# Performance work log

Measured on AMD Instinct MI355X. Metric: run time of the kernel, lower is better.

Reference implementation:

```python
import jax, jax.numpy as jnp
import numpy as np

N, D, O, E = 100000, 32, 64, 1600000

def setup_inputs() -> dict:
    key = jax.random.key(0)
    ks = jax.random.split(key, 6)
    x = jax.random.normal(ks[0], (N, D), dtype=jnp.float32)
    edge_index = jax.random.randint(ks[1], (2, E), 0, N, dtype=jnp.int64)
    edge_attr = jax.random.uniform(ks[2], (E, 1), dtype=jnp.float32)
    # nodec MLP params (stored as [in, out]; equiv to torch Linear weight.T)
    W1 = jax.random.normal(ks[3], (3 * D, O), dtype=jnp.float32) * (1.0 / np.sqrt(3 * D))
    b1 = jnp.zeros((O,), dtype=jnp.float32)
    W2 = jax.random.normal(ks[4], (O, O), dtype=jnp.float32) * (1.0 / np.sqrt(O))
    b2 = jnp.zeros((O,), dtype=jnp.float32)
    return {"x": x, "edge_index": edge_index, "edge_attr": edge_attr,
            "W1": W1, "b1": b1, "W2": W2, "b2": b2}

def reference(x, edge_index, edge_attr, W1, b1, W2, b2):
    row, col = edge_index[0], edge_index[1]
    n = x.shape[0]
    # gather, weight by edge_attr, scatter-add into destination nodes
    mi = jax.ops.segment_sum(edge_attr * x[row], col, num_segments=n)  # [N, D]
    mo = jax.ops.segment_sum(edge_attr * x[col], row, num_segments=n)  # [N, D]
    M = jnp.concatenate([mi, mo, x], axis=-1)  # [N, 3D]
    h = jnp.tanh(M @ W1 + b1)
    return jnp.tanh(h @ W2 + b2)
```

## Files before the change

### kernel.cpp

```cpp
#include <hip/hip_runtime.h>
#include <hip/hip_bf16.h>


#define DFEAT 32
#define OFEAT 64
#define EPB   2048
#define KEYS_PER_BIN 128
#define NBINMAX 1568
#define CAP   3072

typedef unsigned long long u64;

__device__ __forceinline__ float rdlane(float v, int l) {
    return __int_as_float(__builtin_amdgcn_readlane(__float_as_int(v), l));
}

__global__ __launch_bounds__(512) void hist_part(
    const int* __restrict__ ei, int* __restrict__ blockhist, int E, int NBIN)
{
    __shared__ int lh[NBINMAX];
    int blk = blockIdx.x, tid = threadIdx.x;
    for (int i = tid; i < NBIN; i += 512) lh[i] = 0;
    __syncthreads();
    int e0 = blk * EPB;
    if (e0 + EPB <= E) {
        int4 rr = *(const int4*)(ei + e0 + tid * 4);
        int4 cc = *(const int4*)(ei + E + e0 + tid * 4);
        atomicAdd(&lh[(2 * cc.x) >> 7], 1); atomicAdd(&lh[(2 * rr.x + 1) >> 7], 1);
        atomicAdd(&lh[(2 * cc.y) >> 7], 1); atomicAdd(&lh[(2 * rr.y + 1) >> 7], 1);
        atomicAdd(&lh[(2 * cc.z) >> 7], 1); atomicAdd(&lh[(2 * rr.z + 1) >> 7], 1);
        atomicAdd(&lh[(2 * cc.w) >> 7], 1); atomicAdd(&lh[(2 * rr.w + 1) >> 7], 1);
    } else {
        #pragma unroll
        for (int j = 0; j < 4; ++j) {
            int e = e0 + tid * 4 + j;
            if (e < E) {
                atomicAdd(&lh[(2 * ei[E + e]) >> 7], 1);
                atomicAdd(&lh[(2 * ei[e] + 1) >> 7], 1);
            }
        }
    }
    __syncthreads();
    for (int i = tid; i < NBIN; i += 512)
        blockhist[(long long)blk * NBIN + i] = lh[i];
}

__global__ __launch_bounds__(64) void colscan(
    const int* __restrict__ blockhist, int* __restrict__ ofsT,
    int* __restrict__ bintotal, int nPB, int NBIN)
{
    int bin  = blockIdx.x;
    int lane = threadIdx.x;
    int run = 0;
    for (int b0 = 0; b0 < nPB; b0 += 64) {
        int b = b0 + lane;
        int v = (b < nPB) ? blockhist[(long long)b * NBIN + bin] : 0;
        int s = v;
        #pragma unroll
        for (int d = 1; d < 64; d <<= 1) {
            int t = __shfl_up(s, d, 64);
            if (lane >= d) s += t;
        }
        if (b < nPB) ofsT[(long long)bin * nPB + b] = s - v + run;
        run += __shfl(s, 63, 64);
    }
    if (lane == 0) bintotal[bin] = run;
}

__global__ __launch_bounds__(1024) void scan_bins(
    const int* __restrict__ bintotal, int* __restrict__ binbase, int NBIN)
{
    __shared__ int s[1024];
    int t = threadIdx.x;
    int i0 = 2 * t, i1 = 2 * t + 1;
    int p0 = (i0 < NBIN) ? ((bintotal[i0] + 1) & ~1) : 0;
    int p1 = (i1 < NBIN) ? ((bintotal[i1] + 1) & ~1) : 0;
    int v = p0 + p1;
    s[t] = v;
    __syncthreads();
    for (int o = 1; o < 1024; o <<= 1) {
        int u = (t >= o) ? s[t - o] : 0;
        __syncthreads();
        s[t] += u;
        __syncthreads();
    }
    int excl = s[t] - v;
    if (i0 < NBIN) binbase[i0] = excl;
    if (i1 < NBIN) binbase[i1] = excl + p0;
}

__global__ __launch_bounds__(512) void partition_kernel(
    const int* __restrict__ ei, const float* __restrict__ ea,
    const int* __restrict__ ofsT, const int* __restrict__ binbase,
    u64* __restrict__ pay, int E, int NBIN, int nPB)
{
    __shared__ unsigned short lofsw[NBINMAX + 1];
    __shared__ int lcur[NBINMAX];
    __shared__ int lbase[NBINMAX];
    __shared__ u64 stag[2 * EPB];
    int blk = blockIdx.x, tid = threadIdx.x;
    int e0 = blk * EPB;

    for (int i = tid; i < NBIN; i += 512) lcur[i] = 0;
    __syncthreads();

    int4 rr, cc; float4 av; bool full = (e0 + EPB <= E);
    if (full) {
        rr = *(const int4*)(ei + e0 + tid * 4);
        cc = *(const int4*)(ei + E + e0 + tid * 4);
        av = *(const float4*)(ea + e0 + tid * 4);
        atomicAdd(&lcur[(2 * cc.x) >> 7], 1); atomicAdd(&lcur[(2 * rr.x + 1) >> 7], 1);
        atomicAdd(&lcur[(2 * cc.y) >> 7], 1); atomicAdd(&lcur[(2 * rr.y + 1) >> 7], 1);
        atomicAdd(&lcur[(2 * cc.z) >> 7], 1); atomicAdd(&lcur[(2 * rr.z + 1) >> 7], 1);
        atomicAdd(&lcur[(2 * cc.w) >> 7], 1); atomicAdd(&lcur[(2 * rr.w + 1) >> 7], 1);
    } else {
        int rs[4], cs[4]; float as[4];
        #pragma unroll
        for (int j = 0; j < 4; ++j) {
            int e = e0 + tid * 4 + j;
            if (e < E) {
                rs[j] = ei[e]; cs[j] = ei[E + e]; as[j] = ea[e];
                atomicAdd(&lcur[(2 * cs[j]) >> 7], 1);
                atomicAdd(&lcur[(2 * rs[j] + 1) >> 7], 1);
            } else { rs[j] = 0; cs[j] = 0; as[j] = 0.0f; }
        }
        rr = make_int4(rs[0], rs[1], rs[2], rs[3]);
        cc = make_int4(cs[0], cs[1], cs[2], cs[3]);
        av = make_float4(as[0], as[1], as[2], as[3]);
    }
    __syncthreads();

    if (tid < 64) {
        int runc = 0;
        for (int b0 = 0; b0 < NBIN; b0 += 64) {
            int i = b0 + tid;
            int v = (i < NBIN) ? lcur[i] : 0;
            int s = v;
            #pragma unroll
            for (int d = 1; d < 64; d <<= 1) {
                int t2 = __shfl_up(s, d, 64);
                if (tid >= d) s += t2;
            }
            if (i < NBIN) lofsw[i] = (unsigned short)(s - v + runc);
            runc += __shfl(s, 63, 64);
        }
        if (tid == 0) lofsw[NBIN] = (unsigned short)runc;
    }
    __syncthreads();

    for (int i = tid; i < NBIN; i += 512) {
        lcur[i] = 0;
        lbase[i] = binbase[i] + ofsT[(long long)i * nPB + blk];
    }
    __syncthreads();

    {
        int rs[4] = {rr.x, rr.y, rr.z, rr.w};
        int cs[4] = {cc.x, cc.y, cc.z, cc.w};
        float as[4] = {av.x, av.y, av.z, av.w};
        #pragma unroll
        for (int j = 0; j < 4; ++j) {
            int e = e0 + tid * 4 + j;
            if (e < E) {
                unsigned int ab = (unsigned int)__float_as_int(as[j]);
                {
                    int key = 2 * cs[j]; int bin = key >> 7;
                    int t2 = atomicAdd(&lcur[bin], 1);
                    stag[(int)lofsw[bin] + t2] = ((u64)ab << 32) |
                        (unsigned int)(rs[j] | ((key & 127) << 17));
                }
                {
                    int key = 2 * rs[j] + 1; int bin = key >> 7;
                    int t2 = atomicAdd(&lcur[bin], 1);
                    stag[(int)lofsw[bin] + t2] = ((u64)ab << 32) |
                        (unsigned int)(cs[j] | ((key & 127) << 17));
                }
            }
        }
    }
    __syncthreads();

    int total = lofsw[NBIN];
    for (int i = tid; i < total; i += 512) {
        int lo = 0, hi = NBIN;
        while (hi - lo > 1) {
            int mid = (lo + hi) >> 1;
            if ((int)lofsw[mid] <= i) lo = mid; else hi = mid;
        }
        pay[lbase[lo] + (i - (int)lofsw[lo])] = stag[i];
    }
}

__global__ __launch_bounds__(512) void accum_sortgather(
    const float* __restrict__ x,
    const int* __restrict__ binbase, const int* __restrict__ bintotal,
    const u64* __restrict__ pay,
    float* __restrict__ mi, float* __restrict__ mo, int NK)
{
    __shared__ u64 srec[CAP];
    __shared__ int lcnt[KEYS_PER_BIN];
    __shared__ int lofs[KEYS_PER_BIN];
    __shared__ int lcur[KEYS_PER_BIN];

    int b = blockIdx.x, tid = threadIdx.x;
    int base = binbase[b];
    int n    = bintotal[b];
    int wid  = tid >> 6;
    int lane = tid & 63;
    int half = lane >> 5;
    int feat = lane & 31;

    float accA[4], accB[4], accC[4], accD[4];
    #pragma unroll
    for (int p = 0; p < 4; ++p) {
        accA[p] = 0.0f; accB[p] = 0.0f; accC[p] = 0.0f; accD[p] = 0.0f;
    }

    for (int c0 = 0; c0 < n; c0 += CAP) {
        int cn = min(n - c0, CAP);
        if (tid < KEYS_PER_BIN) lcnt[tid] = 0;
        __syncthreads();
        for (int i = tid; i < cn; i += 512)
            atomicAdd(&lcnt[((int)pay[base + c0 + i] >> 17) & 127], 1);
        __syncthreads();
        if (tid < 64) {
            int v0 = lcnt[2 * tid], v1 = lcnt[2 * tid + 1];
            int s = v0 + v1, ss = s;
            #pragma unroll
            for (int d = 1; d < 64; d <<= 1) {
                int t = __shfl_up(ss, d, 64);
                if (tid >= d) ss += t;
            }
            int excl = ss - s;
            lofs[2 * tid] = excl;      lofs[2 * tid + 1] = excl + v0;
            lcur[2 * tid] = excl;      lcur[2 * tid + 1] = excl + v0;
        }
        __syncthreads();
        for (int i = tid; i < cn; i += 512) {
            u64 v = pay[base + c0 + i];
            int t2 = atomicAdd(&lcur[((int)v >> 17) & 127], 1);
            srec[t2] = v;
        }
        __syncthreads();

        #pragma unroll
        for (int p = 0; p < 4; ++p) {
            int kb = wid * 16 + 4 * p;
            int s0 = lofs[kb + 0], e0 = s0 + lcnt[kb + 0];
            int s1 = lofs[kb + 1], e1 = s1 + lcnt[kb + 1];
            int s2 = lofs[kb + 2], e2 = s2 + lcnt[kb + 2];
            int s3 = lofs[kb + 3], e3 = s3 + lcnt[kb + 3];
            int i0 = s0 + half, i1 = s1 + half, i2 = s2 + half, i3 = s3 + half;
            float a0 = accA[p], a1 = accB[p], a2 = accC[p], a3 = accD[p];
            while (i0 < e0 && i1 < e1 && i2 < e2 && i3 < e3) {
                u64 r0 = srec[i0], r1 = srec[i1], r2 = srec[i2], r3 = srec[i3];
                float x0 = x[(long long)((int)r0 & 0x1FFFF) * DFEAT + feat];
                float x1 = x[(long long)((int)r1 & 0x1FFFF) * DFEAT + feat];
                float x2 = x[(long long)((int)r2 & 0x1FFFF) * DFEAT + feat];
                float x3 = x[(long long)((int)r3 & 0x1FFFF) * DFEAT + feat];
                a0 = fmaf(__int_as_float((int)(r0 >> 32)), x0, a0);
                a1 = fmaf(__int_as_float((int)(r1 >> 32)), x1, a1);
                a2 = fmaf(__int_as_float((int)(r2 >> 32)), x2, a2);
                a3 = fmaf(__int_as_float((int)(r3 >> 32)), x3, a3);
                i0 += 2; i1 += 2; i2 += 2; i3 += 2;
            }
            while (i0 < e0) {
                u64 rr = srec[i0];
                a0 = fmaf(__int_as_float((int)(rr >> 32)),
                          x[(long long)((int)rr & 0x1FFFF) * DFEAT + feat], a0);
                i0 += 2;
            }
            while (i1 < e1) {
                u64 rr = srec[i1];
                a1 = fmaf(__int_as_float((int)(rr >> 32)),
                          x[(long long)((int)rr & 0x1FFFF) * DFEAT + feat], a1);
                i1 += 2;
            }
            while (i2 < e2) {
                u64 rr = srec[i2];
                a2 = fmaf(__int_as_float((int)(rr >> 32)),
                          x[(long long)((int)rr & 0x1FFFF) * DFEAT + feat], a2);
                i2 += 2;
            }
            while (i3 < e3) {
                u64 rr = srec[i3];
                a3 = fmaf(__int_as_float((int)(rr >> 32)),
                          x[(long long)((int)rr & 0x1FFFF) * DFEAT + feat], a3);
                i3 += 2;
            }
            accA[p] = a0; accB[p] = a1; accC[p] = a2; accD[p] = a3;
        }
        __syncthreads();
    }

    int key0 = b * KEYS_PER_BIN + wid * 16;
    #pragma unroll
    for (int p = 0; p < 4; ++p) {
        float t0 = accA[p] + __shfl_xor(accA[p], 32, 64);
        float t1 = accB[p] + __shfl_xor(accB[p], 32, 64);
        float t2 = accC[p] + __shfl_xor(accC[p], 32, 64);
        float t3 = accD[p] + __shfl_xor(accD[p], 32, 64);
        float vA = half ? t2 : t0;
        float vB = half ? t3 : t1;
        int gkA = key0 + 4 * p + (half ? 2 : 0);
        int gkB = gkA + 1;
        if (gkA < NK) {
            int node = gkA >> 1;
            ((gkA & 1) ? mo : mi)[(long long)node * DFEAT + feat] = vA;
        }
        if (gkB < NK) {
            int node = gkB >> 1;
            ((gkB & 1) ? mo : mi)[(long long)node * DFEAT + feat] = vB;
        }
    }
}

__global__ __launch_bounds__(256) void edge_scatter_kernel(
    const float* __restrict__ x, const int* __restrict__ ei,
    const float* __restrict__ ea,
    float* __restrict__ mi, float* __restrict__ mo, int E)
{
    long long tid = (long long)blockIdx.x * blockDim.x + threadIdx.x;
    long long total = (long long)E * 8;
    if (tid >= total) return;
    int e = (int)(tid >> 3);
    int q = (int)(tid & 7);
    int r = ei[e];
    int c = ei[E + e];
    float a = ea[e];
    const float4* x4 = (const float4*)x;
    float4 xr = x4[(long long)r * 8 + q];
    float4 xc = x4[(long long)c * 8 + q];
    float* mip = mi + (long long)c * DFEAT + q * 4;
    float* mop = mo + (long long)r * DFEAT + q * 4;
    atomicAdd(mip + 0, a * xr.x); atomicAdd(mip + 1, a * xr.y);
    atomicAdd(mip + 2, a * xr.z); atomicAdd(mip + 3, a * xr.w);
    atomicAdd(mop + 0, a * xc.x); atomicAdd(mop + 1, a * xc.y);
    atomicAdd(mop + 2, a * xc.z); atomicAdd(mop + 3, a * xc.w);
}

__global__ __launch_bounds__(256) void mlp_reg_kernel(
    const float* __restrict__ mi, const float* __restrict__ mo,
    const float* __restrict__ x,
    const float* __restrict__ W1, const float* __restrict__ b1,
    const float* __restrict__ W2, const float* __restrict__ b2,
    float* __restrict__ out, int N)
{
    int o   = threadIdx.x & 63;
    int wid = threadIdx.x >> 6;

    float w1r[96], w2r[64];
    #pragma unroll
    for (int k = 0; k < 96; ++k) w1r[k] = W1[k * 64 + o];
    #pragma unroll
    for (int k = 0; k < 64; ++k) w2r[k] = W2[k * 64 + o];
    float bias1 = b1[o];
    float bias2 = b2[o];

    int stride = gridDim.x * 4;
    for (int node = blockIdx.x * 4 + wid; node < N; node += stride) {
        long long nb = (long long)node * DFEAT;
        float m01 = (o < 32) ? mi[nb + o] : mo[nb + (o - 32)];
        float m2v = (o < 32) ? x[nb + o] : 0.0f;

        float a0 = bias1, a1 = 0.0f, a2 = 0.0f, a3 = 0.0f;
        #pragma unroll
        for (int k = 0; k < 64; k += 4) {
            a0 = fmaf(rdlane(m01, k + 0), w1r[k + 0], a0);
            a1 = fmaf(rdlane(m01, k + 1), w1r[k + 1], a1);
            a2 = fmaf(rdlane(m01, k + 2), w1r[k + 2], a2);
            a3 = fmaf(rdlane(m01, k + 3), w1r[k + 3], a3);
        }
        #pragma unroll
        for (int k = 0; k < 32; k += 4) {
            a0 = fmaf(rdlane(m2v, k + 0), w1r[64 + k + 0], a0);
            a1 = fmaf(rdlane(m2v, k + 1), w1r[64 + k + 1], a1);
            a2 = fmaf(rdlane(m2v, k + 2), w1r[64 + k + 2], a2);
            a3 = fmaf(rdlane(m2v, k + 3), w1r[64 + k + 3], a3);
        }
        float h = tanhf(((a0 + a1) + (a2 + a3)));

        float c0 = bias2, c1 = 0.0f, c2 = 0.0f, c3 = 0.0f;
        #pragma unroll
        for (int k = 0; k < 64; k += 4) {
            c0 = fmaf(rdlane(h, k + 0), w2r[k + 0], c0);
            c1 = fmaf(rdlane(h, k + 1), w2r[k + 1], c1);
            c2 = fmaf(rdlane(h, k + 2), w2r[k + 2], c2);
            c3 = fmaf(rdlane(h, k + 3), w2r[k + 3], c3);
        }
        out[(long long)node * OFEAT + o] = tanhf(((c0 + c1) + (c2 + c3)));
    }
}

extern "C" void kernel_launch(void* const* d_in, const int* in_sizes, int n_in,
                              void* d_out, int out_size, void* d_ws, size_t ws_size,
                              hipStream_t stream) {
    const float* x  = (const float*)d_in[0];
    const int*   ei = (const int*)  d_in[1];
    const float* ea = (const float*)d_in[2];
    const float* W1 = (const float*)d_in[3];
    const float* b1 = (const float*)d_in[4];
    const float* W2 = (const float*)d_in[5];
    const float* b2 = (const float*)d_in[6];
    float* out = (float*)d_out;

    int N    = in_sizes[0] / DFEAT;
    int E    = in_sizes[2];
    int NK   = 2 * N;
    int NBIN = (NK + KEYS_PER_BIN - 1) / KEYS_PER_BIN;
    int nPB  = (E + EPB - 1) / EPB;

    float* mi = (float*)d_ws;
    float* mo = mi + (size_t)N * DFEAT;

    size_t paySlots = (size_t)2 * E + NBIN;
    size_t need = (size_t)N * DFEAT * 2 * 4
                + paySlots * 8
                + (size_t)nPB * NBIN * 4 * 2
                + (size_t)NBIN * 4 * 2 + 64;

    if (ws_size >= need && N <= (1 << 17) && NBIN <= NBINMAX) {
        u64* pay       = (u64*)(mo + (size_t)N * DFEAT);
        int* blockhist = (int*)(pay + paySlots);
        int* ofsT      = blockhist + (size_t)nPB * NBIN;
        int* bintotal  = ofsT + (size_t)nPB * NBIN;
        int* binbase   = bintotal + NBIN;

        hist_part<<<nPB, 512, 0, stream>>>(ei, blockhist, E, NBIN);
        colscan<<<NBIN, 64, 0, stream>>>(blockhist, ofsT, bintotal, nPB, NBIN);
        scan_bins<<<1, 1024, 0, stream>>>(bintotal, binbase, NBIN);
        partition_kernel<<<nPB, 512, 0, stream>>>(ei, ea, ofsT, binbase,
                                                  pay, E, NBIN, nPB);
        accum_sortgather<<<NBIN, 512, 0, stream>>>(x, binbase, bintotal, pay,
                                                   mi, mo, NK);
    } else {
        hipMemsetAsync(d_ws, 0, (size_t)N * DFEAT * 2 * sizeof(float), stream);
        long long total = (long long)E * 8;
        int nblocks = (int)((total + 255) / 256);
        edge_scatter_kernel<<<nblocks, 256, 0, stream>>>(x, ei, ea, mi, mo, E);
    }

    mlp_reg_kernel<<<512, 256, 0, stream>>>(mi, mo, x, W1, b1, W2, b2, out, N);
}
```

Before: 238.7 us.

## Fuse node MLP into sorted-gather accumulation kernel

```diff
diff --git a/kernel.cpp b/kernel.cpp
--- a/kernel.cpp
+++ b/kernel.cpp
@@ -191,11 +191,13 @@
     }
 }
 
-__global__ __launch_bounds__(512) void accum_sortgather(
+__global__ __launch_bounds__(512) void accum_mlp(
     const float* __restrict__ x,
     const int* __restrict__ binbase, const int* __restrict__ bintotal,
     const u64* __restrict__ pay,
-    float* __restrict__ mi, float* __restrict__ mo, int NK)
+    const float* __restrict__ W1, const float* __restrict__ b1,
+    const float* __restrict__ W2, const float* __restrict__ b2,
+    float* __restrict__ out, int NK, int N)
 {
     __shared__ u64 srec[CAP];
     __shared__ int lcnt[KEYS_PER_BIN];
@@ -293,25 +295,72 @@
         __syncthreads();
     }
 
-    int key0 = b * KEYS_PER_BIN + wid * 16;
+    float m01[8];
     #pragma unroll
     for (int p = 0; p < 4; ++p) {
         float t0 = accA[p] + __shfl_xor(accA[p], 32, 64);
         float t1 = accB[p] + __shfl_xor(accB[p], 32, 64);
         float t2 = accC[p] + __shfl_xor(accC[p], 32, 64);
         float t3 = accD[p] + __shfl_xor(accD[p], 32, 64);
-        float vA = half ? t2 : t0;
-        float vB = half ? t3 : t1;
-        int gkA = key0 + 4 * p + (half ? 2 : 0);
-        int gkB = gkA + 1;
-        if (gkA < NK) {
-            int node = gkA >> 1;
-            ((gkA & 1) ? mo : mi)[(long long)node * DFEAT + feat] = vA;
-        }
-        if (gkB < NK) {
-            int node = gkB >> 1;
-            ((gkB & 1) ? mo : mi)[(long long)node * DFEAT + feat] = vB;
-        }
+        m01[2 * p + 0] = half ? t1 : t0;
+        m01[2 * p + 1] = half ? t3 : t2;
+    }
+
+    int o = lane;
+    int node0 = b * 64 + wid * 8;
+    float* wbuf = (float*)srec;
+
+    float m2v[8];
+    #pragma unroll
+    for (int nn = 0; nn < 8; ++nn) {
+        int node = node0 + nn;
+        m2v[nn] = (node < N && o < 32) ? x[(long long)node * DFEAT + o] : 0.0f;
+    }
+
+    __syncthreads();
+    for (int i = tid; i < 96 * 64; i += 512) wbuf[i] = W1[i];
+    __syncthreads();
+
+    float hacc[8];
+    float bias1 = b1[o];
+    #pragma unroll
+    for (int nn = 0; nn < 8; ++nn) hacc[nn] = bias1;
+
+    for (int k = 0; k < 64; ++k) {
+        float w = wbuf[k * 64 + o];
+        #pragma unroll
+        for (int nn = 0; nn < 8; ++nn)
+            hacc[nn] = fmaf(rdlane(m01[nn], k), w, hacc[nn]);
+    }
+    for (int k = 0; k < 32; ++k) {
+        float w = wbuf[(64 + k) * 64 + o];
+        #pragma unroll
+        for (int nn = 0; nn < 8; ++nn)
+            hacc[nn] = fmaf(rdlane(m2v[nn], k), w, hacc[nn]);
+    }
+    #pragma unroll
+    for (int nn = 0; nn < 8; ++nn) hacc[nn] = tanhf(hacc[nn]);
+
+    __syncthreads();
+    for (int i = tid; i < 64 * 64; i += 512) wbuf[i] = W2[i];
+    __syncthreads();
+
+    float oacc[8];
+    float bias2 = b2[o];
+    #pragma unroll
+    for (int nn = 0; nn < 8; ++nn) oacc[nn] = bias2;
+
+    for (int k = 0; k < 64; ++k) {
+        float w = wbuf[k * 64 + o];
+        #pragma unroll
+        for (int nn = 0; nn < 8; ++nn)
+            oacc[nn] = fmaf(rdlane(hacc[nn], k), w, oacc[nn]);
+    }
+    #pragma unroll
+    for (int nn = 0; nn < 8; ++nn) {
+        int node = node0 + nn;
+        if (node < N)
+            out[(long long)node * OFEAT + o] = tanhf(oacc[nn]);
     }
 }
 
@@ -431,14 +480,13 @@
         scan_bins<<<1, 1024, 0, stream>>>(bintotal, binbase, NBIN);
         partition_kernel<<<nPB, 512, 0, stream>>>(ei, ea, ofsT, binbase,
                                                   pay, E, NBIN, nPB);
-        accum_sortgather<<<NBIN, 512, 0, stream>>>(x, binbase, bintotal, pay,
-                                                   mi, mo, NK);
+        accum_mlp<<<NBIN, 512, 0, stream>>>(x, binbase, bintotal, pay,
+                                            W1, b1, W2, b2, out, NK, N);
     } else {
         hipMemsetAsync(d_ws, 0, (size_t)N * DFEAT * 2 * sizeof(float), stream);
         long long total = (long long)E * 8;
         int nblocks = (int)((total + 255) / 256);
         edge_scatter_kernel<<<nblocks, 256, 0, stream>>>(x, ei, ea, mi, mo, E);
-    }
-
-    mlp_reg_kernel<<<512, 256, 0, stream>>>(mi, mo, x, W1, b1, W2, b2, out, N);
-}
+        mlp_reg_kernel<<<512, 256, 0, stream>>>(mi, mo, x, W1, b1, W2, b2, out, N);
+    }
+}
```

Result: slower. 251.4 us (+5.3%).

## Split fused MLP into two register-resident layer kernels via workspace buffer

Applied to the files above, without the earlier changes.

```diff
diff --git a/kernel.cpp b/kernel.cpp
--- a/kernel.cpp
+++ b/kernel.cpp
@@ -315,6 +315,74 @@
     }
 }
 
+__global__ __launch_bounds__(256, 4) void mlp_l1(
+    const float* __restrict__ mi, const float* __restrict__ mo,
+    const float* __restrict__ x,
+    const float* __restrict__ W1, const float* __restrict__ b1,
+    float* __restrict__ hbuf, int N)
+{
+    int o   = threadIdx.x & 63;
+    int wid = threadIdx.x >> 6;
+
+    float w1r[96];
+    #pragma unroll
+    for (int k = 0; k < 96; ++k) w1r[k] = W1[k * 64 + o];
+    float bias1 = b1[o];
+
+    int stride = gridDim.x * 4;
+    for (int node = blockIdx.x * 4 + wid; node < N; node += stride) {
+        long long nb = (long long)node * DFEAT;
+        float m01 = (o < 32) ? mi[nb + o] : mo[nb + (o - 32)];
+        float m2v = (o < 32) ? x[nb + o] : 0.0f;
+
+        float a0 = bias1, a1 = 0.0f, a2 = 0.0f, a3 = 0.0f;
+        #pragma unroll
+        for (int k = 0; k < 64; k += 4) {
+            a0 = fmaf(rdlane(m01, k + 0), w1r[k + 0], a0);
+            a1 = fmaf(rdlane(m01, k + 1), w1r[k + 1], a1);
+            a2 = fmaf(rdlane(m01, k + 2), w1r[k + 2], a2);
+            a3 = fmaf(rdlane(m01, k + 3), w1r[k + 3], a3);
+        }
+        #pragma unroll
+        for (int k = 0; k < 32; k += 4) {
+            a0 = fmaf(rdlane(m2v, k + 0), w1r[64 + k + 0], a0);
+            a1 = fmaf(rdlane(m2v, k + 1), w1r[64 + k + 1], a1);
+            a2 = fmaf(rdlane(m2v, k + 2), w1r[64 + k + 2], a2);
+            a3 = fmaf(rdlane(m2v, k + 3), w1r[64 + k + 3], a3);
+        }
+        hbuf[(long long)node * OFEAT + o] = tanhf(((a0 + a1) + (a2 + a3)));
+    }
+}
+
+__global__ __launch_bounds__(256, 5) void mlp_l2(
+    const float* __restrict__ hbuf,
+    const float* __restrict__ W2, const float* __restrict__ b2,
+    float* __restrict__ out, int N)
+{
+    int o   = threadIdx.x & 63;
+    int wid = threadIdx.x >> 6;
+
+    float w2r[64];
+    #pragma unroll
+    for (int k = 0; k < 64; ++k) w2r[k] = W2[k * 64 + o];
+    float bias2 = b2[o];
+
+    int stride = gridDim.x * 4;
+    for (int node = blockIdx.x * 4 + wid; node < N; node += stride) {
+        float hv = hbuf[(long long)node * OFEAT + o];
+
+        float c0 = bias2, c1 = 0.0f, c2 = 0.0f, c3 = 0.0f;
+        #pragma unroll
+        for (int k = 0; k < 64; k += 4) {
+            c0 = fmaf(rdlane(hv, k + 0), w2r[k + 0], c0);
+            c1 = fmaf(rdlane(hv, k + 1), w2r[k + 1], c1);
+            c2 = fmaf(rdlane(hv, k + 2), w2r[k + 2], c2);
+            c3 = fmaf(rdlane(hv, k + 3), w2r[k + 3], c3);
+        }
+        out[(long long)node * OFEAT + o] = tanhf(((c0 + c1) + (c2 + c3)));
+    }
+}
+
 __global__ __launch_bounds__(256) void edge_scatter_kernel(
     const float* __restrict__ x, const int* __restrict__ ei,
     const float* __restrict__ ea,
@@ -419,7 +487,9 @@
                 + (size_t)nPB * NBIN * 4 * 2
                 + (size_t)NBIN * 4 * 2 + 64;
 
-    if (ws_size >= need && N <= (1 << 17) && NBIN <= NBINMAX) {
+    bool h_fits = (size_t)N * OFEAT * 4 <= paySlots * 8;
+
+    if (ws_size >= need && N <= (1 << 17) && NBIN <= NBINMAX && h_fits) {
         u64* pay       = (u64*)(mo + (size_t)N * DFEAT);
         int* blockhist = (int*)(pay + paySlots);
         int* ofsT      = blockhist + (size_t)nPB * NBIN;
@@ -433,12 +503,14 @@
                                                   pay, E, NBIN, nPB);
         accum_sortgather<<<NBIN, 512, 0, stream>>>(x, binbase, bintotal, pay,
                                                    mi, mo, NK);
+        float* hbuf = (float*)pay;
+        mlp_l1<<<1024, 256, 0, stream>>>(mi, mo, x, W1, b1, hbuf, N);
+        mlp_l2<<<1024, 256, 0, stream>>>(hbuf, W2, b2, out, N);
     } else {
         hipMemsetAsync(d_ws, 0, (size_t)N * DFEAT * 2 * sizeof(float), stream);
         long long total = (long long)E * 8;
         int nblocks = (int)((total + 255) / 256);
         edge_scatter_kernel<<<nblocks, 256, 0, stream>>>(x, ei, ea, mi, mo, E);
-    }
-
-    mlp_reg_kernel<<<512, 256, 0, stream>>>(mi, mo, x, W1, b1, W2, b2, out, N);
-}
+        mlp_reg_kernel<<<512, 256, 0, stream>>>(mi, mo, x, W1, b1, W2, b2, out, N);
+    }
+}
```

Measured after the change: 238.1 us. About the same (-0.2%).
